# Kernel optimization log

Measured on AMD Instinct MI355X. Metric: run time of the kernel, lower is better.

The kernel has to match this reference:

```python
import jax, jax.numpy as jnp
import numpy as np

# dims: B pages, P boxes/page, TOTAL flat boxes, D model, H heads, C coords, Z rel positions, L layers
B, P, TOTAL, D, H, C, Z, L = 16, 512, 6400, 256, 8, 2, 64, 4
HS = D // H          # head size = 32
PAD_COLS = 448       # columns >= PAD_COLS are padding (-1)


def setup_inputs():
    key = jax.random.key(0)
    ks = jax.random.split(key, 10)
    embeds = jax.random.normal(ks[0], (TOTAL, D), jnp.float32)
    page_ids = jax.random.randint(ks[1], (B, P), 0, TOTAL)
    page_ids = page_ids.at[:, PAD_COLS:].set(-1)
    xmin = jax.random.uniform(ks[2], (TOTAL,)) * 0.9
    xmax = xmin + jax.random.uniform(ks[3], (TOTAL,)) * 0.1 + 0.01
    ymin = jax.random.uniform(ks[4], (TOTAL,)) * 0.9
    ymax = ymin + jax.random.uniform(ks[5], (TOTAL,)) * 0.1 + 0.01
    kk = jax.random.split(ks[6], 12)
    w = lambda k, *s: jax.random.normal(k, s, jnp.float32) * 0.02
    return dict(
        embeds=embeds, xmin=xmin, xmax=xmax, ymin=ymin, ymax=ymax,
        width=xmax - xmin, height=ymax - ymin,
        empty_embed=jax.random.normal(ks[7], (D,), jnp.float32),
        position_embedding=jax.random.normal(ks[8], (Z, D), jnp.float32),
        cq_w=w(kk[0], L, D, D), cq_b=jnp.zeros((L, D)),
        ck_w=w(kk[1], L, D, D), ck_b=jnp.zeros((L, D)),
        pk_w=w(kk[2], L, D, D), pk_b=jnp.zeros((L, D)),
        pq_w=w(kk[3], L, D, D), pq_b=jnp.zeros((L, D)),
        cv_w=w(kk[4], L, D, D), cv_b=jnp.zeros((L, D)),
        out_w=w(kk[5], L, D, D), out_b=jnp.zeros((L, D)),
        res1=jnp.full((L,), 0.1, jnp.float32), res2=jnp.full((L,), 0.1, jnp.float32),
        ln1_g=jnp.ones((L, D)), ln1_b=jnp.zeros((L, D)),
        ln2_g=jnp.ones((L, D)), ln2_b=jnp.zeros((L, D)),
        ff1_w=w(kk[6], L, D, 2 * D), ff1_b=jnp.zeros((L, 2 * D)),
        ff2_w=w(kk[7], L, 2 * D, D), ff2_b=jnp.zeros((L, D)),
        page_ids=page_ids,
    )


def _layer_norm(x, g, b, eps=1e-5):
    m = jnp.mean(x, axis=-1, keepdims=True)
    v = jnp.mean((x - m) ** 2, axis=-1, keepdims=True)
    return (x - m) * jax.lax.rsqrt(v + eps) * g + b


def _compute_rel(x0, x1, y0, y1, w, h, n_rel):
    # clamped to +-n_rel//2 and shifted into [0, n_rel)
    cx = (x0 + x1) * 0.5
    cy = (y0 + y1) * 0.5
    dx = jnp.round((cx[:, None, :] - cx[:, :, None]) / jnp.maximum(w[:, :, None], 1e-3))
    dy = jnp.round((cy[:, None, :] - cy[:, :, None]) / jnp.maximum(h[:, :, None], 1e-3))
    half = n_rel // 2
    rel = jnp.stack([dx, dy], axis=-1)
    return (jnp.clip(rel, -half, half - 1) + half).astype(jnp.int32)


def _forward(embeds, xmin, xmax, ymin, ymax, width, height, empty_embed,
             position_embedding, cq_w, cq_b, ck_w, ck_b, pk_w, pk_b, pq_w, pq_b,
             cv_w, cv_b, out_w, out_b, res1, res2, ln1_g, ln1_b, ln2_g, ln2_b,
             ff1_w, ff1_b, ff2_w, ff2_b, page_ids):
    mask = page_ids != -1                                           # [B,P]
    gth = lambda a: a[page_ids]                                     # flat -> [B,P]
    x = jnp.concatenate([jnp.broadcast_to(empty_embed, (B, 1, D)),
                         embeds[page_ids]], axis=1)                 # [B,N,D], N=P+1
    maskc = jnp.concatenate([jnp.ones((B, 1), bool), mask], axis=1) # [B,N]
    rel = _compute_rel(gth(xmin), gth(xmax), gth(ymin), gth(ymax),
                       gth(width), gth(height), Z)                  # [B,P,P,2]
    N = P + 1
    relc = jnp.zeros((B, N, N, 2), jnp.int32).at[:, 1:, 1:, :].set(rel)
    nopos = jnp.ones((B, N, N), bool).at[:, 1:, 1:].set(False)      # disable pos terms on CLS
    scale = 1.0 / float(np.sqrt(HS))
    neg = jnp.finfo(jnp.float32).min

    for l in range(L):
        q = (x @ cq_w[l] + cq_b[l]).reshape(B, N, H, HS)
        k = (x @ ck_w[l] + ck_b[l]).reshape(B, N, H, HS)
        c2c = jnp.einsum('bihd,bjhd->bijh', q, k)                   # [B,N,N,H]
        pk = (position_embedding @ pk_w[l] + pk_b[l]).reshape(Z, C, H, HS // C)
        pq = (position_embedding @ pq_w[l] + pq_b[l]).reshape(Z, C, H, HS // C)
        qc = q.reshape(B, N, H, C, HS // C)
        kc = k.reshape(B, N, H, C, HS // C)
        # c2p: score query against every relative-position key, then gather by index
        c2p = jnp.take_along_axis(jnp.einsum('bihcd,zchd->bizch', qc, pk),
                                  relc[..., None], axis=2)          # [B,N,N,C,H]
        # p2c: score position queries against content keys, gather along position axis
        p2c = jnp.take_along_axis(jnp.einsum('bjhcd,zchd->bzjch', kc, pq),
                                  relc[..., None], axis=1)          # [B,N,N,C,H]
        pos = jnp.sum(c2p + p2c, axis=3) * (~nopos)[..., None].astype(x.dtype)
        logits = (c2c + pos) * scale
        weights = jax.nn.softmax(
            jnp.where(maskc[:, None, :, None], logits, neg), axis=2)
        v = (x @ cv_w[l] + cv_b[l]).reshape(B, N, H, HS)
        upd = jnp.einsum('bijh,bjhd->bihd', weights, v).reshape(B, N, D) @ out_w[l] + out_b[l]
        x = _layer_norm(x + upd * res1[l], ln1_g[l], ln1_b[l])
        ff = jax.nn.gelu(x @ ff1_w[l] + ff1_b[l], approximate=False) @ ff2_w[l] + ff2_b[l]
        x = _layer_norm(x + ff * res2[l], ln2_g[l], ln2_b[l])

    # drop CLS and zero padded boxes (padded static-shape analogue of embeds[:,1:][mask])
    return x[:, 1:] * mask[..., None].astype(x.dtype)


def reference(embeds, xmin, xmax, ymin, ymax, width, height, empty_embed,
              position_embedding, cq_w, cq_b, ck_w, ck_b, pk_w, pk_b, pq_w, pq_b,
              cv_w, cv_b, out_w, out_b, res1, res2, ln1_g, ln1_b, ln2_g, ln2_b,
              ff1_w, ff1_b, ff2_w, ff2_b, page_ids):
    return _forward(embeds, xmin, xmax, ymin, ymax, width, height, empty_embed,
                    position_embedding, cq_w, cq_b, ck_w, ck_b, pk_w, pk_b, pq_w, pq_b,
                    cv_w, cv_b, out_w, out_b, res1, res2, ln1_g, ln1_b, ln2_g, ln2_b,
                    ff1_w, ff1_b, ff2_w, ff2_b, page_ids)
```

## Files before the change

### kernel.cpp

```cpp
#include <hip/hip_runtime.h>
#include <math.h>

#define BB 16
#define PP 512
#define DD 256
#define HH 8
#define NPAD 512
#define NVAL 449
#define MM (BB*PP)
#define NROWS (BB*HH*NPAD)

typedef unsigned short u16;
typedef unsigned u32;
typedef __bf16 v8bf __attribute__((ext_vector_type(8)));
typedef float v4f __attribute__((ext_vector_type(4)));
typedef unsigned short u16x8 __attribute__((ext_vector_type(8)));
typedef unsigned short u16x4 __attribute__((ext_vector_type(4)));

static __device__ __forceinline__ float b2f(u16 u) {
  unsigned v = ((unsigned)u) << 16;
  return __builtin_bit_cast(float, v);
}
static __device__ __forceinline__ u16 f2b(float f) {
  unsigned x = __builtin_bit_cast(unsigned, f);
  unsigned lsb = (x >> 16) & 1u;
  x += 0x7fffu + lsb;
  return (u16)(x >> 16);
}
static __device__ __forceinline__ v8bf ldg8(const u16* p) {
  u16x8 u = *(const u16x8*)p;
  return __builtin_bit_cast(v8bf, u);
}
static __device__ __forceinline__ void gload16(const u16* g, u16* l) {
  __builtin_amdgcn_global_load_lds(
      (__attribute__((address_space(1))) void*)(g),
      (__attribute__((address_space(3))) void*)(l), 16, 0, 0);
}

__global__ void k_prep(const float* embeds, const float* xmin, const float* xmax,
                       const float* ymin, const float* ymax, const float* width,
                       const float* height, const float* empty_embed, const int* page_ids,
                       float* xf, u16* xb, float* gcx, float* gcy, float* gw, float* gh_) {
  int bx = blockIdx.x;
  int b = bx >> 9, r = bx & 511;
  int t = threadIdx.x;
  int c0 = t * 4;
  const float* src = nullptr;
  if (r == 0) src = empty_embed;
  else if (r <= 448) {
    int gi = page_ids[b * PP + (r - 1)];
    src = embeds + (size_t)gi * DD;
  }
  float4 fv = make_float4(0.f, 0.f, 0.f, 0.f);
  if (src) fv = *(const float4*)(src + c0);
  size_t row = (size_t)b * NPAD + r;
  *(float4*)(xf + row * DD + c0) = fv;
  u16x4 bv; bv[0] = f2b(fv.x); bv[1] = f2b(fv.y); bv[2] = f2b(fv.z); bv[3] = f2b(fv.w);
  *(u16x4*)(xb + row * DD + c0) = bv;
  if (t == 0) {
    int p = r;
    int gi = page_ids[b * PP + p];
    float cx = 0.f, cy = 0.f, ww = 1.f, hh = 1.f;
    if (gi >= 0) {
      cx = 0.5f * (xmin[gi] + xmax[gi]);
      cy = 0.5f * (ymin[gi] + ymax[gi]);
      ww = fmaxf(width[gi], 1e-3f);
      hh = fmaxf(height[gi], 1e-3f);
    }
    gcx[b * PP + p] = cx; gcy[b * PP + p] = cy;
    gw[b * PP + p] = ww;  gh_[b * PP + p] = hh;
  }
}

__global__ __launch_bounds__(64) void k_rel(const float* gcx, const float* gcy,
                                            const float* gw, const float* gh_, u16* relp) {
  int bx = blockIdx.x;
  int b = bx >> 9, i = bx & 511;
  int t = threadIdx.x;
  float cxi = 0.f, cyi = 0.f, wi = 1.f, hi = 1.f;
  if (i > 0) {
    cxi = gcx[b * PP + i - 1]; cyi = gcy[b * PP + i - 1];
    wi = gw[b * PP + i - 1];   hi = gh_[b * PP + i - 1];
  }
  u16* dst = relp + ((size_t)b * NPAD + i) * NPAD;
#pragma unroll
  for (int jj = 0; jj < 8; jj++) {
    int j = jj * 64 + t;
    u16 pk = (u16)(32 | (32 << 8));
    if (j > 0) {
      float cxj = gcx[b * PP + j - 1], cyj = gcy[b * PP + j - 1];
      float dxf = rintf((cxj - cxi) / wi);
      float dyf = rintf((cyj - cyi) / hi);
      int zx = (int)(fminf(fmaxf(dxf, -32.f), 31.f)) + 32;
      int zy = (int)(fminf(fmaxf(dyf, -32.f), 31.f)) + 32;
      pk = (u16)(zx | (zy << 8));
    }
    dst[j] = pk;
  }
}

__global__ __launch_bounds__(256) void k_wT(const float* cq, const float* ck, const float* cv,
                                            const float* ow, const float* f1, const float* f2,
                                            u16* wT) {
  __shared__ u16 lds[32][33];
  int bx = blockIdx.x;
  int l = bx >> 9, r = bx & 511;
  const float* src; int N, k0, n0; u16* dst; int dstStride;
  if (r < 192) {
    int mat = r / 64, rr = r % 64;
    k0 = (rr >> 3) * 32; n0 = (rr & 7) * 32;
    src = (mat == 0 ? cq : mat == 1 ? ck : cv) + (size_t)l * 65536;
    N = 256; dst = wT + (size_t)l * 524288 + mat * 65536; dstStride = 256;
  } else if (r < 256) {
    int rr = r - 192;
    k0 = (rr >> 3) * 32; n0 = (rr & 7) * 32;
    src = ow + (size_t)l * 65536; N = 256;
    dst = wT + (size_t)l * 524288 + 196608; dstStride = 256;
  } else if (r < 384) {
    int rr = r - 256;
    k0 = (rr >> 4) * 32; n0 = (rr & 15) * 32;
    src = f1 + (size_t)l * 131072; N = 512;
    dst = wT + (size_t)l * 524288 + 262144; dstStride = 256;
  } else {
    int rr = r - 384;
    k0 = (rr >> 3) * 32; n0 = (rr & 7) * 32;
    src = f2 + (size_t)l * 131072; N = 256;
    dst = wT + (size_t)l * 524288 + 393216; dstStride = 512;
  }
  int tx = threadIdx.x & 31, ty = threadIdx.x >> 5;
#pragma unroll
  for (int yy = 0; yy < 4; yy++) {
    int y = ty + yy * 8;
    lds[y][tx] = f2b(src[(size_t)(k0 + y) * N + n0 + tx]);
  }
  __syncthreads();
#pragma unroll
  for (int yy = 0; yy < 4; yy++) {
    int y = ty + yy * 8;
    dst[(size_t)(n0 + y) * dstStride + k0 + tx] = lds[tx][y];
  }
}

__global__ __launch_bounds__(256) void k_posproj(const float* pe, const float* pkw, const float* pkb,
                                                 const float* pqw, const float* pqb,
                                                 u16* pkfsw, u16* pqfsw) {
  int gid = blockIdx.x * 256 + threadIdx.x;
  int d = gid & 15, z = (gid >> 4) & 63, ch = (gid >> 10) & 15, l = (gid >> 14) & 3, tab = gid >> 16;
  const float* W = (tab ? pqw : pkw) + (size_t)l * 65536;
  const float* Bb = (tab ? pqb : pkb) + (size_t)l * 256;
  int col = (ch >> 3) * 128 + (ch & 7) * 16 + d;
  float s = Bb[col];
  const float* per = pe + (size_t)z * 256;
  for (int kk = 0; kk < 256; kk++) s += per[kk] * W[(size_t)kk * 256 + col];
  u16* dst = tab ? pqfsw : pkfsw;
  dst[(((size_t)l * 16 + ch) * 64 + z) * 16 + d] = f2b(s);
}

template <int EPI>
__global__ __launch_bounds__(256) void k_gemm(const u16* A, const u16* W, int K,
                                              const float* bias0, const float* bias1, const float* bias2,
                                              void* out0, void* out1, void* out2) {
  __shared__ u16 As[2][4096];
  __shared__ u16 Bs[2][4096];
  int w = threadIdx.x >> 6, lane = threadIdx.x & 63;
  int la = lane & 15, lg = lane >> 4;
  int wm = w & 1, wn = w >> 1;
  int m0 = blockIdx.x * 64;
  int n0 = blockIdx.y * 64;
  v4f acc[2][2] = {};
  int nt = K >> 6;
#define STAGE(kb, buf) do {                                                      \
    _Pragma("unroll")                                                            \
    for (int p_ = 0; p_ < 2; p_++) {                                             \
      int e_ = threadIdx.x + p_ * 256;                                           \
      int row_ = e_ >> 3, ch_ = e_ & 7;                                          \
      int sk_ = (ch_ ^ (row_ & 7)) * 8;                                          \
      gload16(A + (size_t)(m0 + row_) * K + (kb) + sk_, &As[buf][e_ * 8]);       \
      gload16(W + (size_t)(n0 + row_) * K + (kb) + sk_, &Bs[buf][e_ * 8]);       \
    }                                                                            \
  } while (0)
  STAGE(0, 0);
  __syncthreads();
  for (int t = 0; t < nt; t++) {
    int cur = t & 1;
    if (t + 1 < nt) STAGE((t + 1) << 6, cur ^ 1);
    const u16* as = As[cur];
    const u16* bs = Bs[cur];
#pragma unroll
    for (int ks = 0; ks < 2; ks++) {
      int ra0 = wm * 32 + la, ra1 = wm * 32 + 16 + la;
      int rb0 = wn * 32 + la, rb1 = wn * 32 + 16 + la;
      v8bf a0 = ldg8(as + ra0 * 64 + ((ks * 32 + lg * 8) ^ ((ra0 & 7) << 3)));
      v8bf a1 = ldg8(as + ra1 * 64 + ((ks * 32 + lg * 8) ^ ((ra1 & 7) << 3)));
      v8bf b0 = ldg8(bs + rb0 * 64 + ((ks * 32 + lg * 8) ^ ((rb0 & 7) << 3)));
      v8bf b1 = ldg8(bs + rb1 * 64 + ((ks * 32 + lg * 8) ^ ((rb1 & 7) << 3)));
      acc[0][0] = __builtin_amdgcn_mfma_f32_16x16x32_bf16(a0, b0, acc[0][0], 0, 0, 0);
      acc[0][1] = __builtin_amdgcn_mfma_f32_16x16x32_bf16(a0, b1, acc[0][1], 0, 0, 0);
      acc[1][0] = __builtin_amdgcn_mfma_f32_16x16x32_bf16(a1, b0, acc[1][0], 0, 0, 0);
      acc[1][1] = __builtin_amdgcn_mfma_f32_16x16x32_bf16(a1, b1, acc[1][1], 0, 0, 0);
    }
    __syncthreads();
  }
#undef STAGE
#pragma unroll
  for (int fi = 0; fi < 2; fi++)
#pragma unroll
    for (int fj = 0; fj < 2; fj++)
#pragma unroll
      for (int rr = 0; rr < 4; rr++) {
        int m = m0 + wm * 32 + fi * 16 + lg * 4 + rr;
        int n = n0 + wn * 32 + fj * 16 + la;
        float v = acc[fi][fj][rr];
        if (EPI == 0) {
          const float* bp = (n < 256 ? bias0 : n < 512 ? bias1 : bias2);
          v += bp[n & 255];
          int b = m >> 9, i = m & 511, h = (n & 255) >> 5, d = n & 31;
          if (n < 512) {
            u16* dst = (u16*)(n < 256 ? out0 : out1);
            dst[(((size_t)(b * 8 + h)) * NPAD + i) * 32 + d] = f2b(v);
          } else {
            ((u16*)out2)[(((size_t)(b * 8 + h)) * 32 + d) * NPAD + i] = f2b(v);
          }
        } else if (EPI == 1) {
          ((u16*)out0)[(size_t)m * 256 + n] = f2b(v + bias0[n]);
        } else {
          float x = v + bias0[n];
          float g = 0.5f * x * (1.0f + erff(x * 0.70710678118654752f));
          ((u16*)out0)[(size_t)m * 512 + n] = f2b(g);
        }
      }
}

__global__ __launch_bounds__(256) void k_gemmA(const u16* opartb, const float* lpart,
                                               const u16* W, const float* bias, u16* y16) {
  __shared__ u16 As[2][4096];
  __shared__ u16 Bs[2][4096];
  int w = threadIdx.x >> 6, lane = threadIdx.x & 63;
  int la = lane & 15, lg = lane >> 4;
  int wm = w & 1, wn = w >> 1;
  int m0 = blockIdx.x * 64;
  int n0 = blockIdx.y * 64;
  v4f acc[2][2] = {};
#define STAGE_A(tt, buf) do {                                                            \
    _Pragma("unroll")                                                                    \
    for (int p_ = 0; p_ < 2; p_++) {                                                     \
      int e_ = threadIdx.x + p_ * 256;                                                   \
      int row_ = e_ >> 3, ch_ = e_ & 7;                                                  \
      int h_ = 2 * (tt) + (ch_ >> 2), dq_ = (ch_ & 3) * 8;                               \
      int m_ = m0 + row_, bb_ = m_ >> 9, ii_ = m_ & 511;                                 \
      size_t rb_ = ((size_t)(bb_ * 8 + h_)) * NPAD + ii_;                                \
      float l_ = lpart[rb_] + lpart[NROWS + rb_] + lpart[2u * NROWS + rb_] + lpart[3u * NROWS + rb_]; \
      float inv_ = 1.0f / l_;                                                            \
      u16x8 a0_ = *(const u16x8*)(opartb + rb_ * 32 + dq_);                              \
      u16x8 a1_ = *(const u16x8*)(opartb + ((size_t)NROWS + rb_) * 32 + dq_);            \
      u16x8 a2_ = *(const u16x8*)(opartb + ((size_t)2u * NROWS + rb_) * 32 + dq_);       \
      u16x8 a3_ = *(const u16x8*)(opartb + ((size_t)3u * NROWS + rb_) * 32 + dq_);       \
      u16x8 r_;                                                                          \
      _Pragma("unroll")                                                                  \
      for (int e2 = 0; e2 < 8; e2++)                                                     \
        r_[e2] = f2b((b2f(a0_[e2]) + b2f(a1_[e2]) + b2f(a2_[e2]) + b2f(a3_[e2])) * inv_);\
      *(u16x8*)(&As[buf][row_ * 64 + ((ch_ ^ (row_ & 7)) * 8)]) = r_;                    \
    }                                                                                    \
  } while (0)
#define STAGE_B(kb, buf) do {                                                    \
    _Pragma("unroll")                                                            \
    for (int p_ = 0; p_ < 2; p_++) {                                             \
      int e_ = threadIdx.x + p_ * 256;                                           \
      int row_ = e_ >> 3, ch_ = e_ & 7;                                          \
      int sk_ = (ch_ ^ (row_ & 7)) * 8;                                          \
      gload16(W + (size_t)(n0 + row_) * 256 + (kb) + sk_, &Bs[buf][e_ * 8]);     \
    }                                                                            \
  } while (0)
  STAGE_A(0, 0);
  STAGE_B(0, 0);
  __syncthreads();
  for (int t = 0; t < 4; t++) {
    int cur = t & 1;
    if (t + 1 < 4) {
      STAGE_A(t + 1, cur ^ 1);
      STAGE_B((t + 1) << 6, cur ^ 1);
    }
    const u16* as = As[cur];
    const u16* bs = Bs[cur];
#pragma unroll
    for (int ks = 0; ks < 2; ks++) {
      int ra0 = wm * 32 + la, ra1 = wm * 32 + 16 + la;
      int rb0 = wn * 32 + la, rb1 = wn * 32 + 16 + la;
      v8bf a0 = ldg8(as + ra0 * 64 + ((ks * 32 + lg * 8) ^ ((ra0 & 7) << 3)));
      v8bf a1 = ldg8(as + ra1 * 64 + ((ks * 32 + lg * 8) ^ ((ra1 & 7) << 3)));
      v8bf b0 = ldg8(bs + rb0 * 64 + ((ks * 32 + lg * 8) ^ ((rb0 & 7) << 3)));
      v8bf b1 = ldg8(bs + rb1 * 64 + ((ks * 32 + lg * 8) ^ ((rb1 & 7) << 3)));
      acc[0][0] = __builtin_amdgcn_mfma_f32_16x16x32_bf16(a0, b0, acc[0][0], 0, 0, 0);
      acc[0][1] = __builtin_amdgcn_mfma_f32_16x16x32_bf16(a0, b1, acc[0][1], 0, 0, 0);
      acc[1][0] = __builtin_amdgcn_mfma_f32_16x16x32_bf16(a1, b0, acc[1][0], 0, 0, 0);
      acc[1][1] = __builtin_amdgcn_mfma_f32_16x16x32_bf16(a1, b1, acc[1][1], 0, 0, 0);
    }
    __syncthreads();
  }
#undef STAGE_A
#undef STAGE_B
#pragma unroll
  for (int fi = 0; fi < 2; fi++)
#pragma unroll
    for (int fj = 0; fj < 2; fj++)
#pragma unroll
      for (int rr = 0; rr < 4; rr++) {
        int mm = m0 + wm * 32 + fi * 16 + lg * 4 + rr;
        int n = n0 + wn * 32 + fj * 16 + la;
        y16[(size_t)mm * 256 + n] = f2b(acc[fi][fj][rr] + bias[n]);
      }
}

__global__ __launch_bounds__(256) void k_tab(const u16* qh, const u16* kh,
                                             const u16* pkfsw, const u16* pqfsw,
                                             u16* tabC2, u16* tabP2, int l) {
  __shared__ __align__(16) u16 qs[4][8][32];
  const u16* srcp = blockIdx.z ? kh : qh;
  const u16* tbl = blockIdx.z ? pqfsw : pkfsw;
  u16* dst = blockIdx.z ? tabP2 : tabC2;
  int b = blockIdx.y, i0 = blockIdx.x * 4;
  int t = threadIdx.x;
  {
    int flat = t * 4;
    int si = flat >> 8, sh = (flat >> 5) & 7, sd = flat & 31;
    *(u16x4*)&qs[si][sh][sd] =
        *(const u16x4*)(srcp + (((size_t)(b * 8 + sh)) * NPAD + i0 + si) * 32 + sd);
  }
  __syncthreads();
  int z = t & 63, cg = t >> 6;
  u16x8 W0[4], W1[4];
#pragma unroll
  for (int cc = 0; cc < 4; cc++) {
    int ch = cg * 4 + cc;
    const u16* pp = tbl + (((size_t)l * 16 + ch) * 64 + z) * 16;
    W0[cc] = *(const u16x8*)pp;
    W1[cc] = *(const u16x8*)(pp + 8);
  }
#pragma unroll
  for (int ii = 0; ii < 4; ii++) {
    u16x4 res;
#pragma unroll
    for (int cc = 0; cc < 4; cc++) {
      int ch = cg * 4 + cc, c = ch >> 3, h = ch & 7;
      const u16* qq = &qs[ii][h][c * 16];
      float s = 0.f;
#pragma unroll
      for (int d = 0; d < 8; d++) s += b2f(qq[d]) * b2f(W0[cc][d]);
#pragma unroll
      for (int d = 0; d < 8; d++) s += b2f(qq[d + 8]) * b2f(W1[cc][d]);
      res[cc] = f2b(s);
    }
    *(u16x4*)&dst[(((size_t)b * NPAD + i0 + ii) * 64 + z) * 16 + cg * 4] = res;
  }
}

__global__ __launch_bounds__(512) void k_attn(const u16* qh, const u16* kh, const u16* vtp,
                                              const u16* tabC2, const u16* tabP2, const u16* relp,
                                              u16* opartb, float* lpart) {
  __shared__ u32 posb[4][16][68];
  __shared__ __align__(16) u16 ps[8][16][72];
  int bid = blockIdx.x;
  int idx = (bid & 7) * 256 + (bid >> 3);
  int b = idx >> 7;
  int rest = idx & 127;
  int i0 = (rest >> 2) * 16;
  int part = rest & 3;
  int t = threadIdx.x, w = t >> 6, lane = t & 63;
  int la = lane & 15, lg = lane >> 4;
  v8bf qa = ldg8(qh + (((size_t)(b * 8 + w)) * NPAD + i0 + la) * 32 + lg * 8);
  float lrow[4] = {0.f, 0.f, 0.f, 0.f};
  v4f o0 = {}; v4f o1 = {};
  const float scale = 0.17677669529663687f;
  const float MC = 8.0f;
  const u16* kbase = kh + ((size_t)(b * 8 + w)) * NPAD * 32;
  const u16* vbase = vtp + ((size_t)(b * 8 + w)) * 32 * NPAD;
  const u16* rbase = relp + ((size_t)b * NPAD + i0) * NPAD;
  int ntile = (part == 3) ? 1 : 2;
  u16x8 Av[2], Bv[2], Cv[2], Dv[2];
  bool fval[2];
#define FETCH(J0) do {                                                          \
    _Pragma("unroll")                                                           \
    for (int pp = 0; pp < 2; pp++) {                                            \
      int p_ = t + pp * 512;                                                    \
      int si_ = p_ >> 6, sj_ = p_ & 63;                                         \
      int ig_ = i0 + si_, jg_ = (J0) + sj_;                                     \
      bool v_ = (ig_ > 0 && jg_ > 0);                                           \
      fval[pp] = v_;                                                            \
      if (v_) {                                                                 \
        unsigned rp_ = rbase[(size_t)si_ * NPAD + jg_];                         \
        int zx_ = rp_ & 255, zy_ = rp_ >> 8;                                    \
        Av[pp] = *(const u16x8*)(tabC2 + (((size_t)b * NPAD + ig_) * 64 + zx_) * 16);     \
        Cv[pp] = *(const u16x8*)(tabP2 + (((size_t)b * NPAD + jg_) * 64 + zx_) * 16);     \
        Bv[pp] = *(const u16x8*)(tabC2 + (((size_t)b * NPAD + ig_) * 64 + zy_) * 16 + 8); \
        Dv[pp] = *(const u16x8*)(tabP2 + (((size_t)b * NPAD + jg_) * 64 + zy_) * 16 + 8); \
      }                                                                         \
    }                                                                           \
  } while (0)
  FETCH(part * 128);
  for (int tt = 0; tt < ntile; tt++) {
    int j0 = (part * 2 + tt) * 64;
#pragma unroll
    for (int pp = 0; pp < 2; pp++) {
      int p = t + pp * 512;
      int si = p >> 6, sj = p & 63;
      float pos[8] = {0.f, 0.f, 0.f, 0.f, 0.f, 0.f, 0.f, 0.f};
      if (fval[pp]) {
#pragma unroll
        for (int h = 0; h < 8; h++)
          pos[h] = (b2f(Av[pp][h]) + b2f(Cv[pp][h])) + (b2f(Bv[pp][h]) + b2f(Dv[pp][h]));
      }
#pragma unroll
      for (int hp = 0; hp < 4; hp++)
        posb[hp][si][sj] = (u32)f2b(pos[2 * hp]) | ((u32)f2b(pos[2 * hp + 1]) << 16);
    }
    __syncthreads();
    v4f s[4];
#pragma unroll
    for (int fj = 0; fj < 4; fj++) {
      v8bf kf = ldg8(kbase + (size_t)(j0 + fj * 16 + la) * 32 + lg * 8);
      v4f zero = {};
      s[fj] = __builtin_amdgcn_mfma_f32_16x16x32_bf16(qa, kf, zero, 0, 0, 0);
    }
    float pvv[4][4];
    int wsel = (w & 1) ? 16 : 0;
#pragma unroll
    for (int fj = 0; fj < 4; fj++) {
#pragma unroll
      for (int rr = 0; rr < 4; rr++) {
        int il = lg * 4 + rr;
        u32 pk = posb[w >> 1][il][fj * 16 + la];
        float posv = b2f((u16)(pk >> wsel));
        float lv = (s[fj][rr] + posv) * scale;
        pvv[fj][rr] = __expf(lv - MC);
      }
    }
    __syncthreads();
    if (tt + 1 < ntile) FETCH(j0 + 64);
#pragma unroll
    for (int rr = 0; rr < 4; rr++)
      lrow[rr] += pvv[0][rr] + pvv[1][rr] + pvv[2][rr] + pvv[3][rr];
#pragma unroll
    for (int fj = 0; fj < 4; fj++)
#pragma unroll
      for (int rr = 0; rr < 4; rr++)
        ps[w][lg * 4 + rr][fj * 16 + la] = f2b(pvv[fj][rr]);
    v8bf pa0 = __builtin_bit_cast(v8bf, *(const u16x8*)&ps[w][la][lg * 8]);
    v8bf pa1 = __builtin_bit_cast(v8bf, *(const u16x8*)&ps[w][la][32 + lg * 8]);
    v8bf v00 = ldg8(vbase + (size_t)la * NPAD + j0 + lg * 8);
    v8bf v01 = ldg8(vbase + (size_t)la * NPAD + j0 + 32 + lg * 8);
    v8bf v10 = ldg8(vbase + (size_t)(16 + la) * NPAD + j0 + lg * 8);
    v8bf v11 = ldg8(vbase + (size_t)(16 + la) * NPAD + j0 + 32 + lg * 8);
    o0 = __builtin_amdgcn_mfma_f32_16x16x32_bf16(pa0, v00, o0, 0, 0, 0);
    o0 = __builtin_amdgcn_mfma_f32_16x16x32_bf16(pa1, v01, o0, 0, 0, 0);
    o1 = __builtin_amdgcn_mfma_f32_16x16x32_bf16(pa0, v10, o1, 0, 0, 0);
    o1 = __builtin_amdgcn_mfma_f32_16x16x32_bf16(pa1, v11, o1, 0, 0, 0);
  }
#undef FETCH
  if (part == 3) {
    v8bf kf = ldg8(kbase + (size_t)448 * 32 + lg * 8);
    float dot = 0.f;
#pragma unroll
    for (int e = 0; e < 8; e++) dot += (float)qa[e] * (float)kf[e];
    dot += __shfl_xor(dot, 16);
    dot += __shfl_xor(dot, 32);
    int ig = i0 + la;
    float pos = 0.f;
    if (ig > 0) {
      unsigned rp = relp[((size_t)b * NPAD + ig) * NPAD + 448];
      int zx = rp & 255, zy = rp >> 8;
      pos = b2f(tabC2[(((size_t)b * NPAD + ig) * 64 + zx) * 16 + w])
          + b2f(tabP2[(((size_t)b * NPAD + 448) * 64 + zx) * 16 + w])
          + b2f(tabC2[(((size_t)b * NPAD + ig) * 64 + zy) * 16 + 8 + w])
          + b2f(tabP2[(((size_t)b * NPAD + 448) * 64 + zy) * 16 + 8 + w]);
    }
    float p448 = __expf((dot + pos) * scale - MC);
    float va = b2f(vbase[(size_t)la * NPAD + 448]);
    float vb_ = b2f(vbase[(size_t)(16 + la) * NPAD + 448]);
#pragma unroll
    for (int rr = 0; rr < 4; rr++) {
      float pr = __shfl(p448, lg * 4 + rr);
      o0[rr] += pr * va;
      o1[rr] += pr * vb_;
      if (la == 0) lrow[rr] += pr;
    }
  }
#pragma unroll
  for (int rr = 0; rr < 4; rr++) {
    float l = lrow[rr];
    l += __shfl_xor(l, 1); l += __shfl_xor(l, 2); l += __shfl_xor(l, 4); l += __shfl_xor(l, 8);
    int ig = i0 + lg * 4 + rr;
    size_t row = (size_t)part * NROWS + (((size_t)(b * 8 + w)) * NPAD + ig);
    opartb[row * 32 + la] = f2b(o0[rr]);
    opartb[row * 32 + 16 + la] = f2b(o1[rr]);
    if (la == 0) lpart[row] = l;
  }
}

template <int LAST>
__global__ __launch_bounds__(256) void k_ln(float* xf, u16* xb, const u16* y16,
                                            const float* resv, int ridx,
                                            const float* g_, const float* b_, float* outp) {
  int row = blockIdx.x * 4 + (threadIdx.x >> 6);
  int lane = threadIdx.x & 63;
  float res = resv[ridx];
  const u16* yr = y16 + (size_t)row * DD;
  float* xr = xf + (size_t)row * DD;
  int c = lane * 4;
  float4 xv = *(const float4*)(xr + c);
  u16x4 yv = *(const u16x4*)(yr + c);
  float v0 = xv.x + b2f(yv[0]) * res, v1 = xv.y + b2f(yv[1]) * res;
  float v2 = xv.z + b2f(yv[2]) * res, v3 = xv.w + b2f(yv[3]) * res;
  float sum = v0 + v1 + v2 + v3;
  sum += __shfl_xor(sum, 1); sum += __shfl_xor(sum, 2); sum += __shfl_xor(sum, 4);
  sum += __shfl_xor(sum, 8); sum += __shfl_xor(sum, 16); sum += __shfl_xor(sum, 32);
  float mean = sum * (1.0f / 256.0f);
  float d0 = v0 - mean, d1 = v1 - mean, d2 = v2 - mean, d3 = v3 - mean;
  float vs = d0 * d0 + d1 * d1 + d2 * d2 + d3 * d3;
  vs += __shfl_xor(vs, 1); vs += __shfl_xor(vs, 2); vs += __shfl_xor(vs, 4);
  vs += __shfl_xor(vs, 8); vs += __shfl_xor(vs, 16); vs += __shfl_xor(vs, 32);
  float rstd = rsqrtf(vs * (1.0f / 256.0f) + 1e-5f);
  float o0 = d0 * rstd * g_[c + 0] + b_[c + 0];
  float o1 = d1 * rstd * g_[c + 1] + b_[c + 1];
  float o2 = d2 * rstd * g_[c + 2] + b_[c + 2];
  float o3 = d3 * rstd * g_[c + 3] + b_[c + 3];
  if (!LAST) {
    *(float4*)(xr + c) = make_float4(o0, o1, o2, o3);
    u16x4 bv; bv[0] = f2b(o0); bv[1] = f2b(o1); bv[2] = f2b(o2); bv[3] = f2b(o3);
    *(u16x4*)(xb + (size_t)row * DD + c) = bv;
  } else {
    int bq = row >> 9, r = row & 511;
    if (r >= 1) {
      int p = r - 1;
      float4 val = (p < 448) ? make_float4(o0, o1, o2, o3) : make_float4(0.f, 0.f, 0.f, 0.f);
      *(float4*)(outp + ((size_t)bq * PP + p) * DD + c) = val;
    } else {
      *(float4*)(outp + ((size_t)bq * PP + 511) * DD + c) = make_float4(0.f, 0.f, 0.f, 0.f);
    }
  }
}

__global__ void k_diag(float* out, int v) {
  int gid = blockIdx.x * 64 + threadIdx.x;
  float4 r = make_float4(0.f, 0.f, 0.f, 0.f);
  if (gid == 28672) r.x = (float)v;
  *(float4*)(out + (size_t)gid * 4) = r;
}

extern "C" void kernel_launch(void* const* d_in, const int* in_sizes, int n_in,
                              void* d_out, int out_size, void* d_ws, size_t ws_size,
                              hipStream_t stream) {
  const float* embeds = (const float*)d_in[0];
  const float* xmin = (const float*)d_in[1];
  const float* xmax = (const float*)d_in[2];
  const float* ymin = (const float*)d_in[3];
  const float* ymax = (const float*)d_in[4];
  const float* width = (const float*)d_in[5];
  const float* height = (const float*)d_in[6];
  const float* empty_embed = (const float*)d_in[7];
  const float* pos_emb = (const float*)d_in[8];
  const float* cq_w = (const float*)d_in[9];
  const float* cq_b = (const float*)d_in[10];
  const float* ck_w = (const float*)d_in[11];
  const float* ck_b = (const float*)d_in[12];
  const float* pk_w = (const float*)d_in[13];
  const float* pk_b = (const float*)d_in[14];
  const float* pq_w = (const float*)d_in[15];
  const float* pq_b = (const float*)d_in[16];
  const float* cv_w = (const float*)d_in[17];
  const float* cv_b = (const float*)d_in[18];
  const float* out_w = (const float*)d_in[19];
  const float* out_b = (const float*)d_in[20];
  const float* res1 = (const float*)d_in[21];
  const float* res2 = (const float*)d_in[22];
  const float* ln1_g = (const float*)d_in[23];
  const float* ln1_b = (const float*)d_in[24];
  const float* ln2_g = (const float*)d_in[25];
  const float* ln2_b = (const float*)d_in[26];
  const float* ff1_w = (const float*)d_in[27];
  const float* ff1_b = (const float*)d_in[28];
  const float* ff2_w = (const float*)d_in[29];
  const float* ff2_b = (const float*)d_in[30];
  const int* page_ids = (const int*)d_in[31];

  char* ws = (char*)d_ws;
  size_t off = 0;
  auto alloc = [&](size_t bytes) -> void* {
    void* p = ws + off;
    off += (bytes + 255) & ~(size_t)255;
    return p;
  };
  float* xf = (float*)alloc((size_t)MM * DD * 4);
  u16* xb = (u16*)alloc((size_t)MM * DD * 2);
  u16* qh = (u16*)alloc((size_t)MM * DD * 2);
  u16* kh = (u16*)alloc((size_t)MM * DD * 2);
  u16* vt = (u16*)alloc((size_t)MM * DD * 2);
  u16* y16 = (u16*)alloc((size_t)MM * DD * 2);
  u16* h1b = (u16*)alloc((size_t)MM * 512 * 2);
  u16* tabC2 = (u16*)alloc((size_t)BB * NPAD * 64 * 16 * 2);
  u16* tabP2 = (u16*)alloc((size_t)BB * NPAD * 64 * 16 * 2);
  u16* relp = (u16*)alloc((size_t)BB * NPAD * NPAD * 2);
  u16* opartb = (u16*)alloc((size_t)4 * NROWS * 32 * 2);
  float* lpart = (float*)alloc((size_t)4 * NROWS * 4);
  u16* wT = (u16*)alloc((size_t)4 * 524288 * 2);
  u16* pkfsw = (u16*)alloc((size_t)4 * 16 * 64 * 16 * 2);
  u16* pqfsw = (u16*)alloc((size_t)4 * 16 * 64 * 16 * 2);
  float* gcx = (float*)alloc((size_t)BB * PP * 4);
  float* gcy = (float*)alloc((size_t)BB * PP * 4);
  float* gw = (float*)alloc((size_t)BB * PP * 4);
  float* gh_ = (float*)alloc((size_t)BB * PP * 4);
  (void)in_sizes; (void)n_in; (void)out_size;

  if (off > ws_size) {
    k_diag<<<dim3(8192), 64, 0, stream>>>((float*)d_out, 216);
    return;
  }

  k_prep<<<dim3(8192), 64, 0, stream>>>(embeds, xmin, xmax, ymin, ymax, width, height,
                                        empty_embed, page_ids, xf, xb, gcx, gcy, gw, gh_);
  k_rel<<<dim3(8192), 64, 0, stream>>>(gcx, gcy, gw, gh_, relp);
  k_wT<<<dim3(2048), 256, 0, stream>>>(cq_w, ck_w, cv_w, out_w, ff1_w, ff2_w, wT);
  k_posproj<<<dim3(512), 256, 0, stream>>>(pos_emb, pk_w, pk_b, pq_w, pq_b, pkfsw, pqfsw);

  for (int l = 0; l < 4; l++) {
    const u16* wl = wT + (size_t)l * 524288;
    k_gemm<0><<<dim3(128, 12), 256, 0, stream>>>(xb, wl, 256, cq_b + l * 256, ck_b + l * 256,
                                                 cv_b + l * 256, qh, kh, vt);
    k_tab<<<dim3(128, 16, 2), 256, 0, stream>>>(qh, kh, pkfsw, pqfsw, tabC2, tabP2, l);
    k_attn<<<dim3(2048), 512, 0, stream>>>(qh, kh, vt, tabC2, tabP2, relp, opartb, lpart);
    k_gemmA<<<dim3(128, 4), 256, 0, stream>>>(opartb, lpart, wl + 196608, out_b + l * 256, y16);
    k_ln<0><<<dim3(2048), 256, 0, stream>>>(xf, xb, y16, res1, l, ln1_g + l * 256, ln1_b + l * 256,
                                            (float*)d_out);
    k_gemm<2><<<dim3(128, 8), 256, 0, stream>>>(xb, wl + 262144, 256, ff1_b + l * 512,
                                                nullptr, nullptr, h1b, nullptr, nullptr);
    k_gemm<1><<<dim3(128, 4), 256, 0, stream>>>(h1b, wl + 393216, 512, ff2_b + l * 256,
                                                nullptr, nullptr, y16, nullptr, nullptr);
    if (l < 3)
      k_ln<0><<<dim3(2048), 256, 0, stream>>>(xf, xb, y16, res2, l, ln2_g + l * 256,
                                              ln2_b + l * 256, (float*)d_out);
    else
      k_ln<1><<<dim3(2048), 256, 0, stream>>>(xf, xb, y16, res2, l, ln2_g + l * 256,
                                              ln2_b + l * 256, (float*)d_out);
  }
}
```

Measured before the change: 536.1 us.

## Template GEMM on M-tile size and batch attention positional fetch up front

The GEMM kernel takes an M-tile parameter, and the QKV and FF1 GEMMs use 128-row tiles with half the blocks, so each weight tile is reused across more rows. In attention, the positional bias for both j-tiles is gathered into a larger shared buffer before a single barrier. This replaces the software-prefetched FETCH pipeline and its per-tile barriers. The trade-offs are more shared memory and accumulators per block, fewer GEMM blocks, and gather latency that is no longer overlapped with MFMA work.

```diff
diff --git a/kernel.cpp b/kernel.cpp
--- a/kernel.cpp
+++ b/kernel.cpp
@@ -156,26 +156,35 @@
   dst[(((size_t)l * 16 + ch) * 64 + z) * 16 + d] = f2b(s);
 }
 
-template <int EPI>
+template <int EPI, int BM>
 __global__ __launch_bounds__(256) void k_gemm(const u16* A, const u16* W, int K,
                                               const float* bias0, const float* bias1, const float* bias2,
                                               void* out0, void* out1, void* out2) {
-  __shared__ u16 As[2][4096];
+  constexpr int WROWS = BM / 2;
+  constexpr int FI = WROWS / 16;
+  constexpr int ACH = BM / 32;
+  __shared__ u16 As[2][BM * 64];
   __shared__ u16 Bs[2][4096];
   int w = threadIdx.x >> 6, lane = threadIdx.x & 63;
   int la = lane & 15, lg = lane >> 4;
   int wm = w & 1, wn = w >> 1;
-  int m0 = blockIdx.x * 64;
+  int m0 = blockIdx.x * BM;
   int n0 = blockIdx.y * 64;
-  v4f acc[2][2] = {};
+  v4f acc[FI][2] = {};
   int nt = K >> 6;
 #define STAGE(kb, buf) do {                                                      \
+    _Pragma("unroll")                                                            \
+    for (int p_ = 0; p_ < ACH; p_++) {                                           \
+      int e_ = threadIdx.x + p_ * 256;                                           \
+      int row_ = e_ >> 3, ch_ = e_ & 7;                                          \
+      int sk_ = (ch_ ^ (row_ & 7)) * 8;                                          \
+      gload16(A + (size_t)(m0 + row_) * K + (kb) + sk_, &As[buf][e_ * 8]);       \
+    }                                                                            \
     _Pragma("unroll")                                                            \
     for (int p_ = 0; p_ < 2; p_++) {                                             \
       int e_ = threadIdx.x + p_ * 256;                                           \
       int row_ = e_ >> 3, ch_ = e_ & 7;                                          \
       int sk_ = (ch_ ^ (row_ & 7)) * 8;                                          \
-      gload16(A + (size_t)(m0 + row_) * K + (kb) + sk_, &As[buf][e_ * 8]);       \
       gload16(W + (size_t)(n0 + row_) * K + (kb) + sk_, &Bs[buf][e_ * 8]);       \
     }                                                                            \
   } while (0)
@@ -188,27 +197,31 @@
     const u16* bs = Bs[cur];
 #pragma unroll
     for (int ks = 0; ks < 2; ks++) {
-      int ra0 = wm * 32 + la, ra1 = wm * 32 + 16 + la;
+      v8bf af[FI];
+#pragma unroll
+      for (int fi = 0; fi < FI; fi++) {
+        int ra = wm * WROWS + fi * 16 + la;
+        af[fi] = ldg8(as + ra * 64 + ((ks * 32 + lg * 8) ^ ((ra & 7) << 3)));
+      }
       int rb0 = wn * 32 + la, rb1 = wn * 32 + 16 + la;
-      v8bf a0 = ldg8(as + ra0 * 64 + ((ks * 32 + lg * 8) ^ ((ra0 & 7) << 3)));
-      v8bf a1 = ldg8(as + ra1 * 64 + ((ks * 32 + lg * 8) ^ ((ra1 & 7) << 3)));
       v8bf b0 = ldg8(bs + rb0 * 64 + ((ks * 32 + lg * 8) ^ ((rb0 & 7) << 3)));
       v8bf b1 = ldg8(bs + rb1 * 64 + ((ks * 32 + lg * 8) ^ ((rb1 & 7) << 3)));
-      acc[0][0] = __builtin_amdgcn_mfma_f32_16x16x32_bf16(a0, b0, acc[0][0], 0, 0, 0);
-      acc[0][1] = __builtin_amdgcn_mfma_f32_16x16x32_bf16(a0, b1, acc[0][1], 0, 0, 0);
-      acc[1][0] = __builtin_amdgcn_mfma_f32_16x16x32_bf16(a1, b0, acc[1][0], 0, 0, 0);
-      acc[1][1] = __builtin_amdgcn_mfma_f32_16x16x32_bf16(a1, b1, acc[1][1], 0, 0, 0);
+#pragma unroll
+      for (int fi = 0; fi < FI; fi++) {
+        acc[fi][0] = __builtin_amdgcn_mfma_f32_16x16x32_bf16(af[fi], b0, acc[fi][0], 0, 0, 0);
+        acc[fi][1] = __builtin_amdgcn_mfma_f32_16x16x32_bf16(af[fi], b1, acc[fi][1], 0, 0, 0);
+      }
     }
     __syncthreads();
   }
 #undef STAGE
 #pragma unroll
-  for (int fi = 0; fi < 2; fi++)
+  for (int fi = 0; fi < FI; fi++)
 #pragma unroll
     for (int fj = 0; fj < 2; fj++)
 #pragma unroll
       for (int rr = 0; rr < 4; rr++) {
-        int m = m0 + wm * 32 + fi * 16 + lg * 4 + rr;
+        int m = m0 + wm * WROWS + fi * 16 + lg * 4 + rr;
         int n = n0 + wn * 32 + fj * 16 + la;
         float v = acc[fi][fj][rr];
         if (EPI == 0) {
@@ -357,7 +370,7 @@
 __global__ __launch_bounds__(512) void k_attn(const u16* qh, const u16* kh, const u16* vtp,
                                               const u16* tabC2, const u16* tabP2, const u16* relp,
                                               u16* opartb, float* lpart) {
-  __shared__ u32 posb[4][16][68];
+  __shared__ u32 posb[4][16][134];
   __shared__ __align__(16) u16 ps[8][16][72];
   int bid = blockIdx.x;
   int idx = (bid & 7) * 256 + (bid >> 3);
@@ -376,44 +389,33 @@
   const u16* vbase = vtp + ((size_t)(b * 8 + w)) * 32 * NPAD;
   const u16* rbase = relp + ((size_t)b * NPAD + i0) * NPAD;
   int ntile = (part == 3) ? 1 : 2;
-  u16x8 Av[2], Bv[2], Cv[2], Dv[2];
-  bool fval[2];
-#define FETCH(J0) do {                                                          \
-    _Pragma("unroll")                                                           \
-    for (int pp = 0; pp < 2; pp++) {                                            \
-      int p_ = t + pp * 512;                                                    \
-      int si_ = p_ >> 6, sj_ = p_ & 63;                                         \
-      int ig_ = i0 + si_, jg_ = (J0) + sj_;                                     \
-      bool v_ = (ig_ > 0 && jg_ > 0);                                           \
-      fval[pp] = v_;                                                            \
-      if (v_) {                                                                 \
-        unsigned rp_ = rbase[(size_t)si_ * NPAD + jg_];                         \
-        int zx_ = rp_ & 255, zy_ = rp_ >> 8;                                    \
-        Av[pp] = *(const u16x8*)(tabC2 + (((size_t)b * NPAD + ig_) * 64 + zx_) * 16);     \
-        Cv[pp] = *(const u16x8*)(tabP2 + (((size_t)b * NPAD + jg_) * 64 + zx_) * 16);     \
-        Bv[pp] = *(const u16x8*)(tabC2 + (((size_t)b * NPAD + ig_) * 64 + zy_) * 16 + 8); \
-        Dv[pp] = *(const u16x8*)(tabP2 + (((size_t)b * NPAD + jg_) * 64 + zy_) * 16 + 8); \
-      }                                                                         \
-    }                                                                           \
-  } while (0)
-  FETCH(part * 128);
   for (int tt = 0; tt < ntile; tt++) {
     int j0 = (part * 2 + tt) * 64;
 #pragma unroll
     for (int pp = 0; pp < 2; pp++) {
       int p = t + pp * 512;
       int si = p >> 6, sj = p & 63;
+      int ig = i0 + si, jg = j0 + sj;
       float pos[8] = {0.f, 0.f, 0.f, 0.f, 0.f, 0.f, 0.f, 0.f};
-      if (fval[pp]) {
+      if (ig > 0 && jg > 0) {
+        unsigned rp = rbase[(size_t)si * NPAD + jg];
+        int zx = rp & 255, zy = rp >> 8;
+        u16x8 Av = *(const u16x8*)(tabC2 + (((size_t)b * NPAD + ig) * 64 + zx) * 16);
+        u16x8 Cv = *(const u16x8*)(tabP2 + (((size_t)b * NPAD + jg) * 64 + zx) * 16);
+        u16x8 Bv = *(const u16x8*)(tabC2 + (((size_t)b * NPAD + ig) * 64 + zy) * 16 + 8);
+        u16x8 Dv = *(const u16x8*)(tabP2 + (((size_t)b * NPAD + jg) * 64 + zy) * 16 + 8);
 #pragma unroll
         for (int h = 0; h < 8; h++)
-          pos[h] = (b2f(Av[pp][h]) + b2f(Cv[pp][h])) + (b2f(Bv[pp][h]) + b2f(Dv[pp][h]));
+          pos[h] = (b2f(Av[h]) + b2f(Cv[h])) + (b2f(Bv[h]) + b2f(Dv[h]));
       }
 #pragma unroll
       for (int hp = 0; hp < 4; hp++)
-        posb[hp][si][sj] = (u32)f2b(pos[2 * hp]) | ((u32)f2b(pos[2 * hp + 1]) << 16);
-    }
-    __syncthreads();
+        posb[hp][si][tt * 66 + sj] = (u32)f2b(pos[2 * hp]) | ((u32)f2b(pos[2 * hp + 1]) << 16);
+    }
+  }
+  __syncthreads();
+  for (int tt = 0; tt < ntile; tt++) {
+    int j0 = (part * 2 + tt) * 64;
     v4f s[4];
 #pragma unroll
     for (int fj = 0; fj < 4; fj++) {
@@ -428,14 +430,12 @@
 #pragma unroll
       for (int rr = 0; rr < 4; rr++) {
         int il = lg * 4 + rr;
-        u32 pk = posb[w >> 1][il][fj * 16 + la];
+        u32 pk = posb[w >> 1][il][tt * 66 + fj * 16 + la];
         float posv = b2f((u16)(pk >> wsel));
         float lv = (s[fj][rr] + posv) * scale;
         pvv[fj][rr] = __expf(lv - MC);
       }
     }
-    __syncthreads();
-    if (tt + 1 < ntile) FETCH(j0 + 64);
 #pragma unroll
     for (int rr = 0; rr < 4; rr++)
       lrow[rr] += pvv[0][rr] + pvv[1][rr] + pvv[2][rr] + pvv[3][rr];
@@ -455,7 +455,6 @@
     o1 = __builtin_amdgcn_mfma_f32_16x16x32_bf16(pa0, v10, o1, 0, 0, 0);
     o1 = __builtin_amdgcn_mfma_f32_16x16x32_bf16(pa1, v11, o1, 0, 0, 0);
   }
-#undef FETCH
   if (part == 3) {
     v8bf kf = ldg8(kbase + (size_t)448 * 32 + lg * 8);
     float dot = 0.f;
@@ -623,17 +622,17 @@
 
   for (int l = 0; l < 4; l++) {
     const u16* wl = wT + (size_t)l * 524288;
-    k_gemm<0><<<dim3(128, 12), 256, 0, stream>>>(xb, wl, 256, cq_b + l * 256, ck_b + l * 256,
-                                                 cv_b + l * 256, qh, kh, vt);
+    k_gemm<0, 128><<<dim3(64, 12), 256, 0, stream>>>(xb, wl, 256, cq_b + l * 256, ck_b + l * 256,
+                                                     cv_b + l * 256, qh, kh, vt);
     k_tab<<<dim3(128, 16, 2), 256, 0, stream>>>(qh, kh, pkfsw, pqfsw, tabC2, tabP2, l);
     k_attn<<<dim3(2048), 512, 0, stream>>>(qh, kh, vt, tabC2, tabP2, relp, opartb, lpart);
     k_gemmA<<<dim3(128, 4), 256, 0, stream>>>(opartb, lpart, wl + 196608, out_b + l * 256, y16);
     k_ln<0><<<dim3(2048), 256, 0, stream>>>(xf, xb, y16, res1, l, ln1_g + l * 256, ln1_b + l * 256,
                                             (float*)d_out);
-    k_gemm<2><<<dim3(128, 8), 256, 0, stream>>>(xb, wl + 262144, 256, ff1_b + l * 512,
-                                                nullptr, nullptr, h1b, nullptr, nullptr);
-    k_gemm<1><<<dim3(128, 4), 256, 0, stream>>>(h1b, wl + 393216, 512, ff2_b + l * 256,
-                                                nullptr, nullptr, y16, nullptr, nullptr);
+    k_gemm<2, 128><<<dim3(64, 8), 256, 0, stream>>>(xb, wl + 262144, 256, ff1_b + l * 512,
+                                                    nullptr, nullptr, h1b, nullptr, nullptr);
+    k_gemm<1, 64><<<dim3(128, 4), 256, 0, stream>>>(h1b, wl + 393216, 512, ff2_b + l * 256,
+                                                    nullptr, nullptr, y16, nullptr, nullptr);
     if (l < 3)
       k_ln<0><<<dim3(2048), 256, 0, stream>>>(xf, xb, y16, res2, l, ln2_g + l * 256,
                                               ln2_b + l * 256, (float*)d_out);
```

After: 541.0 us. About the same (+0.9%).

## Drop split-K attention partials; each block covers all keys and normalizes in place

Applied to the files above, without the earlier changes.

The attention kernel no longer splits the key range into four parts. Each block now loops over all seven 64-key tiles and writes the normalized per-head output directly in row-major bf16. The partial-output and partial-sum buffers go away, and so does the custom output-projection GEMM that merged them, which is replaced by the generic k_gemm<1>. The aim is to cut partial-buffer traffic and the combine work. In exchange, attention runs only 512 blocks instead of 2048, which lowers parallelism and latency hiding.

```diff
diff --git a/kernel.cpp b/kernel.cpp
--- a/kernel.cpp
+++ b/kernel.cpp
@@ -231,86 +231,6 @@
       }
 }
 
-__global__ __launch_bounds__(256) void k_gemmA(const u16* opartb, const float* lpart,
-                                               const u16* W, const float* bias, u16* y16) {
-  __shared__ u16 As[2][4096];
-  __shared__ u16 Bs[2][4096];
-  int w = threadIdx.x >> 6, lane = threadIdx.x & 63;
-  int la = lane & 15, lg = lane >> 4;
-  int wm = w & 1, wn = w >> 1;
-  int m0 = blockIdx.x * 64;
-  int n0 = blockIdx.y * 64;
-  v4f acc[2][2] = {};
-#define STAGE_A(tt, buf) do {                                                            \
-    _Pragma("unroll")                                                                    \
-    for (int p_ = 0; p_ < 2; p_++) {                                                     \
-      int e_ = threadIdx.x + p_ * 256;                                                   \
-      int row_ = e_ >> 3, ch_ = e_ & 7;                                                  \
-      int h_ = 2 * (tt) + (ch_ >> 2), dq_ = (ch_ & 3) * 8;                               \
-      int m_ = m0 + row_, bb_ = m_ >> 9, ii_ = m_ & 511;                                 \
-      size_t rb_ = ((size_t)(bb_ * 8 + h_)) * NPAD + ii_;                                \
-      float l_ = lpart[rb_] + lpart[NROWS + rb_] + lpart[2u * NROWS + rb_] + lpart[3u * NROWS + rb_]; \
-      float inv_ = 1.0f / l_;                                                            \
-      u16x8 a0_ = *(const u16x8*)(opartb + rb_ * 32 + dq_);                              \
-      u16x8 a1_ = *(const u16x8*)(opartb + ((size_t)NROWS + rb_) * 32 + dq_);            \
-      u16x8 a2_ = *(const u16x8*)(opartb + ((size_t)2u * NROWS + rb_) * 32 + dq_);       \
-      u16x8 a3_ = *(const u16x8*)(opartb + ((size_t)3u * NROWS + rb_) * 32 + dq_);       \
-      u16x8 r_;                                                                          \
-      _Pragma("unroll")                                                                  \
-      for (int e2 = 0; e2 < 8; e2++)                                                     \
-        r_[e2] = f2b((b2f(a0_[e2]) + b2f(a1_[e2]) + b2f(a2_[e2]) + b2f(a3_[e2])) * inv_);\
-      *(u16x8*)(&As[buf][row_ * 64 + ((ch_ ^ (row_ & 7)) * 8)]) = r_;                    \
-    }                                                                                    \
-  } while (0)
-#define STAGE_B(kb, buf) do {                                                    \
-    _Pragma("unroll")                                                            \
-    for (int p_ = 0; p_ < 2; p_++) {                                             \
-      int e_ = threadIdx.x + p_ * 256;                                           \
-      int row_ = e_ >> 3, ch_ = e_ & 7;                                          \
-      int sk_ = (ch_ ^ (row_ & 7)) * 8;                                          \
-      gload16(W + (size_t)(n0 + row_) * 256 + (kb) + sk_, &Bs[buf][e_ * 8]);     \
-    }                                                                            \
-  } while (0)
-  STAGE_A(0, 0);
-  STAGE_B(0, 0);
-  __syncthreads();
-  for (int t = 0; t < 4; t++) {
-    int cur = t & 1;
-    if (t + 1 < 4) {
-      STAGE_A(t + 1, cur ^ 1);
-      STAGE_B((t + 1) << 6, cur ^ 1);
-    }
-    const u16* as = As[cur];
-    const u16* bs = Bs[cur];
-#pragma unroll
-    for (int ks = 0; ks < 2; ks++) {
-      int ra0 = wm * 32 + la, ra1 = wm * 32 + 16 + la;
-      int rb0 = wn * 32 + la, rb1 = wn * 32 + 16 + la;
-      v8bf a0 = ldg8(as + ra0 * 64 + ((ks * 32 + lg * 8) ^ ((ra0 & 7) << 3)));
-      v8bf a1 = ldg8(as + ra1 * 64 + ((ks * 32 + lg * 8) ^ ((ra1 & 7) << 3)));
-      v8bf b0 = ldg8(bs + rb0 * 64 + ((ks * 32 + lg * 8) ^ ((rb0 & 7) << 3)));
-      v8bf b1 = ldg8(bs + rb1 * 64 + ((ks * 32 + lg * 8) ^ ((rb1 & 7) << 3)));
-      acc[0][0] = __builtin_amdgcn_mfma_f32_16x16x32_bf16(a0, b0, acc[0][0], 0, 0, 0);
-      acc[0][1] = __builtin_amdgcn_mfma_f32_16x16x32_bf16(a0, b1, acc[0][1], 0, 0, 0);
-      acc[1][0] = __builtin_amdgcn_mfma_f32_16x16x32_bf16(a1, b0, acc[1][0], 0, 0, 0);
-      acc[1][1] = __builtin_amdgcn_mfma_f32_16x16x32_bf16(a1, b1, acc[1][1], 0, 0, 0);
-    }
-    __syncthreads();
-  }
-#undef STAGE_A
-#undef STAGE_B
-#pragma unroll
-  for (int fi = 0; fi < 2; fi++)
-#pragma unroll
-    for (int fj = 0; fj < 2; fj++)
-#pragma unroll
-      for (int rr = 0; rr < 4; rr++) {
-        int mm = m0 + wm * 32 + fi * 16 + lg * 4 + rr;
-        int n = n0 + wn * 32 + fj * 16 + la;
-        y16[(size_t)mm * 256 + n] = f2b(acc[fi][fj][rr] + bias[n]);
-      }
-}
-
 __global__ __launch_bounds__(256) void k_tab(const u16* qh, const u16* kh,
                                              const u16* pkfsw, const u16* pqfsw,
                                              u16* tabC2, u16* tabP2, int l) {
@@ -356,15 +276,13 @@
 
 __global__ __launch_bounds__(512) void k_attn(const u16* qh, const u16* kh, const u16* vtp,
                                               const u16* tabC2, const u16* tabP2, const u16* relp,
-                                              u16* opartb, float* lpart) {
+                                              u16* updb) {
   __shared__ u32 posb[4][16][68];
   __shared__ __align__(16) u16 ps[8][16][72];
   int bid = blockIdx.x;
-  int idx = (bid & 7) * 256 + (bid >> 3);
-  int b = idx >> 7;
-  int rest = idx & 127;
-  int i0 = (rest >> 2) * 16;
-  int part = rest & 3;
+  int idx = (bid & 7) * 64 + (bid >> 3);
+  int b = idx >> 5;
+  int i0 = (idx & 31) * 16;
   int t = threadIdx.x, w = t >> 6, lane = t & 63;
   int la = lane & 15, lg = lane >> 4;
   v8bf qa = ldg8(qh + (((size_t)(b * 8 + w)) * NPAD + i0 + la) * 32 + lg * 8);
@@ -375,7 +293,6 @@
   const u16* kbase = kh + ((size_t)(b * 8 + w)) * NPAD * 32;
   const u16* vbase = vtp + ((size_t)(b * 8 + w)) * 32 * NPAD;
   const u16* rbase = relp + ((size_t)b * NPAD + i0) * NPAD;
-  int ntile = (part == 3) ? 1 : 2;
   u16x8 Av[2], Bv[2], Cv[2], Dv[2];
   bool fval[2];
 #define FETCH(J0) do {                                                          \
@@ -396,9 +313,9 @@
       }                                                                         \
     }                                                                           \
   } while (0)
-  FETCH(part * 128);
-  for (int tt = 0; tt < ntile; tt++) {
-    int j0 = (part * 2 + tt) * 64;
+  FETCH(0);
+  for (int tt = 0; tt < 7; tt++) {
+    int j0 = tt * 64;
 #pragma unroll
     for (int pp = 0; pp < 2; pp++) {
       int p = t + pp * 512;
@@ -435,7 +352,7 @@
       }
     }
     __syncthreads();
-    if (tt + 1 < ntile) FETCH(j0 + 64);
+    if (tt + 1 < 7) FETCH(j0 + 64);
 #pragma unroll
     for (int rr = 0; rr < 4; rr++)
       lrow[rr] += pvv[0][rr] + pvv[1][rr] + pvv[2][rr] + pvv[3][rr];
@@ -456,7 +373,7 @@
     o1 = __builtin_amdgcn_mfma_f32_16x16x32_bf16(pa1, v11, o1, 0, 0, 0);
   }
 #undef FETCH
-  if (part == 3) {
+  {
     v8bf kf = ldg8(kbase + (size_t)448 * 32 + lg * 8);
     float dot = 0.f;
 #pragma unroll
@@ -488,11 +405,11 @@
   for (int rr = 0; rr < 4; rr++) {
     float l = lrow[rr];
     l += __shfl_xor(l, 1); l += __shfl_xor(l, 2); l += __shfl_xor(l, 4); l += __shfl_xor(l, 8);
+    float inv = 1.0f / l;
     int ig = i0 + lg * 4 + rr;
-    size_t row = (size_t)part * NROWS + (((size_t)(b * 8 + w)) * NPAD + ig);
-    opartb[row * 32 + la] = f2b(o0[rr]);
-    opartb[row * 32 + 16 + la] = f2b(o1[rr]);
-    if (la == 0) lpart[row] = l;
+    size_t base = ((size_t)b * NPAD + ig) * DD + w * 32;
+    updb[base + la] = f2b(o0[rr] * inv);
+    updb[base + 16 + la] = f2b(o1[rr] * inv);
   }
 }
 
@@ -594,13 +511,12 @@
   u16* qh = (u16*)alloc((size_t)MM * DD * 2);
   u16* kh = (u16*)alloc((size_t)MM * DD * 2);
   u16* vt = (u16*)alloc((size_t)MM * DD * 2);
+  u16* updb = (u16*)alloc((size_t)MM * DD * 2);
   u16* y16 = (u16*)alloc((size_t)MM * DD * 2);
   u16* h1b = (u16*)alloc((size_t)MM * 512 * 2);
   u16* tabC2 = (u16*)alloc((size_t)BB * NPAD * 64 * 16 * 2);
   u16* tabP2 = (u16*)alloc((size_t)BB * NPAD * 64 * 16 * 2);
   u16* relp = (u16*)alloc((size_t)BB * NPAD * NPAD * 2);
-  u16* opartb = (u16*)alloc((size_t)4 * NROWS * 32 * 2);
-  float* lpart = (float*)alloc((size_t)4 * NROWS * 4);
   u16* wT = (u16*)alloc((size_t)4 * 524288 * 2);
   u16* pkfsw = (u16*)alloc((size_t)4 * 16 * 64 * 16 * 2);
   u16* pqfsw = (u16*)alloc((size_t)4 * 16 * 64 * 16 * 2);
@@ -626,8 +542,9 @@
     k_gemm<0><<<dim3(128, 12), 256, 0, stream>>>(xb, wl, 256, cq_b + l * 256, ck_b + l * 256,
                                                  cv_b + l * 256, qh, kh, vt);
     k_tab<<<dim3(128, 16, 2), 256, 0, stream>>>(qh, kh, pkfsw, pqfsw, tabC2, tabP2, l);
-    k_attn<<<dim3(2048), 512, 0, stream>>>(qh, kh, vt, tabC2, tabP2, relp, opartb, lpart);
-    k_gemmA<<<dim3(128, 4), 256, 0, stream>>>(opartb, lpart, wl + 196608, out_b + l * 256, y16);
+    k_attn<<<dim3(512), 512, 0, stream>>>(qh, kh, vt, tabC2, tabP2, relp, updb);
+    k_gemm<1><<<dim3(128, 4), 256, 0, stream>>>(updb, wl + 196608, 256, out_b + l * 256,
+                                                nullptr, nullptr, y16, nullptr, nullptr);
     k_ln<0><<<dim3(2048), 256, 0, stream>>>(xf, xb, y16, res1, l, ln1_g + l * 256, ln1_b + l * 256,
                                             (float*)d_out);
     k_gemm<2><<<dim3(128, 8), 256, 0, stream>>>(xb, wl + 262144, 256, ff1_b + l * 512,
```

New measurement: 501.7 us. -6.4%, faster.
